# Kernel optimization log

Measured on AMD Instinct MI355X. Metric: run time of the kernel, lower is better.

Reference implementation:

```python
import jax, jax.numpy as jnp
import numpy as np


def setup_inputs() -> dict:
    key = jax.random.key(0)
    ks = jax.random.split(key, 7)
    B, N, F, H = 128, 64, 128, 128
    s1 = 1.0 / np.sqrt(2 * N)  # torch Linear default-ish scaling
    s2 = 1.0 / np.sqrt(H)
    return {
        "agent_features": jax.random.normal(ks[0], (B, N, F), dtype=jnp.float32),
        "W1": jax.random.normal(ks[1], (2 * N, H), dtype=jnp.float32) * s1,
        "b1": jax.random.normal(ks[2], (H,), dtype=jnp.float32) * s1,
        "W2": jax.random.normal(ks[3], (H, H), dtype=jnp.float32) * s2,
        "b2": jax.random.normal(ks[4], (H,), dtype=jnp.float32) * s2,
        "w3": jax.random.normal(ks[5], (H,), dtype=jnp.float32) * s2,
        "b3": jax.random.normal(ks[6], (1,), dtype=jnp.float32) * s2,
        "mixing_weights": jnp.ones((N,), dtype=jnp.float32) / N,
    }


def reference(agent_features, W1, b1, W2, b2, w3, b3, mixing_weights):
    N = mixing_weights.shape[0]
    f = agent_features[:, :, :N]  # [B, N, N] (first num_agents features)
    # Split first Linear's weight into the i-half and j-half of the concat:
    # concat([f_i, f_j]) @ W1 == f_i @ W1[:N] + f_j @ W1[N:]
    Ai = jnp.einsum('bnf,fh->bnh', f, W1[:N])   # contribution of agent i
    Aj = jnp.einsum('bnf,fh->bnh', f, W1[N:])   # contribution of agent j
    h1 = jax.nn.relu(Ai[:, :, None, :] + Aj[:, None, :, :] + b1)  # [B,N,N,H]
    h2 = jax.nn.relu(jnp.einsum('bijh,hk->bijk', h1, W2) + b2)    # [B,N,N,H]
    correlations = jax.nn.sigmoid(jnp.einsum('bijh,h->bij', h2, w3) + b3[0])
    weights = jax.nn.softmax(mixing_weights, axis=0)
    return correlations, weights
```

## Files before the change

### kernel.cpp

```cpp
#include <hip/hip_runtime.h>
#include <hip/hip_bf16.h>


typedef __bf16 bf16x8 __attribute__((ext_vector_type(8)));
typedef float f32x4 __attribute__((ext_vector_type(4)));

__device__ __forceinline__ unsigned rne16(float x) {
  unsigned u = __float_as_uint(x);
  u += 0x7fffu + ((u >> 16) & 1u);
  return u >> 16;
}
__device__ __forceinline__ __bf16 us_as_bf16(unsigned short s) {
  union { unsigned short s; __bf16 h; } cv; cv.s = s; return cv.h;
}

__global__ __launch_bounds__(512, 4) void fused_kernel(
    const float* __restrict__ af, const float* __restrict__ W1,
    const float* __restrict__ b1, const float* __restrict__ W2,
    const float* __restrict__ b2, const float* __restrict__ w3,
    const float* __restrict__ b3, const float* __restrict__ mw,
    float* __restrict__ out)
{
  __shared__ __align__(16) unsigned short W2s[128 * 128];
  __bf16* const flh = (__bf16*)W2s;
  __bf16* const fll = flh + 64 * 72;
  __shared__ __align__(16) float AjF[64 * 132];
  __shared__ __align__(16) float AiF[16 * 132];
  __shared__ float b2s[128], w3s[128];
  __shared__ float part[2][2][128];

  const int tid  = threadIdx.x;
  const int lane = tid & 63;
  const int wave = tid >> 6;
  const int c = lane & 15, g = lane >> 4;
  const int wm = wave & 1;
  const int wn = wave >> 1;

  const int blk = blockIdx.x;
  const int b   = blk >> 2;
  const int iq  = blk & 3;
  const int ip0 = iq << 3;

  if (blk == 0 && tid < 64) {
    float v = mw[tid];
    float m = v;
    for (int off = 32; off > 0; off >>= 1) m = fmaxf(m, __shfl_xor(m, off));
    float e = expf(v - m);
    float s = e;
    for (int off = 32; off > 0; off >>= 1) s += __shfl_xor(s, off);
    out[128 * 64 * 64 + tid] = e / s;
  }

  {
    const float4* srcQ = (const float4*)(af + (b << 13));
#pragma unroll
    for (int p = 0; p < 2; ++p) {
      const int idx = (p << 9) + tid;
      const int n = idx >> 4, e = idx & 15;
      const float4 v = srcQ[(n << 5) + e];
      const unsigned h0 = rne16(v.x), h1 = rne16(v.y),
                     h2 = rne16(v.z), h3 = rne16(v.w);
      const unsigned l0 = rne16(v.x - __uint_as_float(h0 << 16));
      const unsigned l1 = rne16(v.y - __uint_as_float(h1 << 16));
      const unsigned l2 = rne16(v.z - __uint_as_float(h2 << 16));
      const unsigned l3 = rne16(v.w - __uint_as_float(h3 << 16));
      uint2 ph; ph.x = h0 | (h1 << 16); ph.y = h2 | (h3 << 16);
      uint2 pl; pl.x = l0 | (l1 << 16); pl.y = l2 | (l3 << 16);
      *(uint2*)&flh[n * 72 + (e << 2)] = ph;
      *(uint2*)&fll[n * 72 + (e << 2)] = pl;
    }
    if (tid < 128) b2s[tid] = b2[tid];
    else if (tid < 256) w3s[tid - 128] = w3[tid - 128];
  }

  const float bias3 = b3[0];

  __syncthreads();

  {
    const int w = wave;
    bf16x8 ajh[2], ajl[2], aih[2], ail[2];
#pragma unroll
    for (int kc = 0; kc < 2; ++kc) {
      const float* wpj = W1 + ((64 + (kc << 5) + (g << 3)) << 7) + (w << 4) + c;
      const float* wpi = W1 + (((kc << 5) + (g << 3)) << 7) + (w << 4) + c;
#pragma unroll
      for (int e = 0; e < 8; ++e) {
        const float vj = wpj[e << 7];
        const unsigned hj = rne16(vj);
        ajh[kc][e] = us_as_bf16((unsigned short)hj);
        ajl[kc][e] = us_as_bf16((unsigned short)rne16(vj - __uint_as_float(hj << 16)));
        const float vi = wpi[e << 7];
        const unsigned hi_ = rne16(vi);
        aih[kc][e] = us_as_bf16((unsigned short)hi_);
        ail[kc][e] = us_as_bf16((unsigned short)rne16(vi - __uint_as_float(hi_ << 16)));
      }
    }
#pragma unroll
    for (int rt = 0; rt < 4; ++rt) {
      const __bf16* bp = &flh[((rt << 4) + c) * 72 + (g << 3)];
      const __bf16* bq = &fll[((rt << 4) + c) * 72 + (g << 3)];
      f32x4 acc = {0.f, 0.f, 0.f, 0.f};
#pragma unroll
      for (int kc = 0; kc < 2; ++kc) {
        const bf16x8 bh = *(const bf16x8*)(bp + (kc << 5));
        const bf16x8 bl = *(const bf16x8*)(bq + (kc << 5));
        acc = __builtin_amdgcn_mfma_f32_16x16x32_bf16(ajh[kc], bh, acc, 0, 0, 0);
        acc = __builtin_amdgcn_mfma_f32_16x16x32_bf16(ajh[kc], bl, acc, 0, 0, 0);
        acc = __builtin_amdgcn_mfma_f32_16x16x32_bf16(ajl[kc], bh, acc, 0, 0, 0);
      }
      *(f32x4*)&AjF[((rt << 4) + c) * 132 + (w << 4) + (g << 2)] = acc;
    }
    {
      const __bf16* bp = &flh[((iq << 4) + c) * 72 + (g << 3)];
      const __bf16* bq = &fll[((iq << 4) + c) * 72 + (g << 3)];
      f32x4 acc = *(const f32x4*)(b1 + (w << 4) + (g << 2));
#pragma unroll
      for (int kc = 0; kc < 2; ++kc) {
        const bf16x8 bh = *(const bf16x8*)(bp + (kc << 5));
        const bf16x8 bl = *(const bf16x8*)(bq + (kc << 5));
        acc = __builtin_amdgcn_mfma_f32_16x16x32_bf16(aih[kc], bh, acc, 0, 0, 0);
        acc = __builtin_amdgcn_mfma_f32_16x16x32_bf16(aih[kc], bl, acc, 0, 0, 0);
        acc = __builtin_amdgcn_mfma_f32_16x16x32_bf16(ail[kc], bh, acc, 0, 0, 0);
      }
      *(f32x4*)&AiF[c * 132 + (w << 4) + (g << 2)] = acc;
    }
  }

  __syncthreads();

  {
    const int ktw = wn;
#pragma unroll
    for (int mt = 0; mt < 4; ++mt) {
      const int m = (wm << 6) + (mt << 4) + c;
      const float* wp = W2 + (((ktw << 5) + (g << 3)) << 7) + m;
      bf16x8 v;
#pragma unroll
      for (int e = 0; e < 8; ++e) {
        const float vv = wp[e << 7];
        v[e] = us_as_bf16((unsigned short)rne16(vv));
      }
      *(bf16x8*)&W2s[(m << 7) + ((((ktw << 2) + g) ^ c) << 3)] = v;
    }
  }

  f32x4 ajr[4][2][2];
#pragma unroll
  for (int kt = 0; kt < 4; ++kt)
#pragma unroll
    for (int tn = 0; tn < 2; ++tn) {
      const int j = ((wn << 5) + (tn << 4) + c) & 63;
      const float* ajb = &AjF[j * 132 + (g << 3) + (kt << 5)];
      ajr[kt][tn][0] = *(const f32x4*)(ajb);
      ajr[kt][tn][1] = *(const f32x4*)(ajb + 4);
    }

  __syncthreads();

  const int i_sel = wn >> 1;

  for (int t = 0; t < 8; ++t) {
    const float* aib = &AiF[((t << 1) + i_sel) * 132 + (g << 3)];

    f32x4 acc[4][2];
#pragma unroll
    for (int mt = 0; mt < 4; ++mt) {
      const f32x4 bv = *(const f32x4*)&b2s[(wm << 6) + (mt << 4) + (g << 2)];
      acc[mt][0] = bv;
      acc[mt][1] = bv;
    }

#pragma unroll
    for (int kt = 0; kt < 4; ++kt) {
      const int es = ((kt << 2) + g) ^ c;
      bf16x8 wv[4];
#pragma unroll
      for (int mt = 0; mt < 4; ++mt)
        wv[mt] = *(const bf16x8*)&W2s[(((wm << 6) + (mt << 4) + c) << 7) + (es << 3)];

      const f32x4 a0 = *(const f32x4*)(aib + (kt << 5));
      const f32x4 a1 = *(const f32x4*)(aib + (kt << 5) + 4);
      bf16x8 hv[2];
#pragma unroll
      for (int tn = 0; tn < 2; ++tn) {
        const f32x4 h0  = a0 + ajr[kt][tn][0];
        const f32x4 h1v = a1 + ajr[kt][tn][1];
#pragma unroll
        for (int e = 0; e < 4; ++e) {
          hv[tn][e]     = (__bf16)fmaxf(h0[e], 0.f);
          hv[tn][e + 4] = (__bf16)fmaxf(h1v[e], 0.f);
        }
      }
#pragma unroll
      for (int mt = 0; mt < 4; ++mt)
#pragma unroll
        for (int tn = 0; tn < 2; ++tn)
          acc[mt][tn] = __builtin_amdgcn_mfma_f32_16x16x32_bf16(
              wv[mt], hv[tn], acc[mt][tn], 0, 0, 0);
    }

    float s0 = 0.f, s1 = 0.f;
#pragma unroll
    for (int mt = 0; mt < 4; ++mt) {
      const f32x4 wv3 = *(const f32x4*)&w3s[(wm << 6) + (mt << 4) + (g << 2)];
#pragma unroll
      for (int p = 0; p < 4; ++p) {
        s0 = fmaf(fmaxf(acc[mt][0][p], 0.f), wv3[p], s0);
        s1 = fmaf(fmaxf(acc[mt][1][p], 0.f), wv3[p], s1);
      }
    }
    s0 += __shfl_xor(s0, 16);
    s0 += __shfl_xor(s0, 32);
    s1 += __shfl_xor(s1, 16);
    s1 += __shfl_xor(s1, 32);

    const int pb = t & 1;
    if (g == 0) {
      part[pb][wm][(wn << 5) + c]      = s0;
      part[pb][wm][(wn << 5) + 16 + c] = s1;
    }

    __syncthreads();

    if (tid < 128) {
      const float v = part[pb][0][tid] + part[pb][1][tid] + bias3;
      out[(b << 12) + ((ip0 + t) << 7) + tid] = 1.f / (1.f + __expf(-v));
    }
  }
}

extern "C" void kernel_launch(void* const* d_in, const int* in_sizes, int n_in,
                              void* d_out, int out_size, void* d_ws,
                              size_t ws_size, hipStream_t stream)
{
  const float* af = (const float*)d_in[0];
  const float* W1 = (const float*)d_in[1];
  const float* b1 = (const float*)d_in[2];
  const float* W2 = (const float*)d_in[3];
  const float* b2 = (const float*)d_in[4];
  const float* w3 = (const float*)d_in[5];
  const float* b3 = (const float*)d_in[6];
  const float* mw = (const float*)d_in[7];
  float* out = (float*)d_out;

  (void)d_ws; (void)ws_size;
  fused_kernel<<<512, 512, 0, stream>>>(af, W1, b1, W2, b2, w3, b3, mw, out);
}
```

Baseline: 95.32 us.

## Keep W2 fragments in registers and remap waves to process sixteen rows per block

Each wave now holds its bf16 W2 slice (32 output channels across all K tiles) in registers, so the per-iteration LDS reads of W2 and the W2 shared-memory staging are gone. Waves are remapped to a 4×2 split over output channels and columns. Each block walks its 16 i-rows in groups of four, with one barrier and a four-way partial reduction per group, which cuts the number of barriers. The cost is extra register pressure (W2 fragments plus cached Aj values) under the launch bound, which could cause spills or lower occupancy.

```diff
diff --git a/kernel.cpp b/kernel.cpp
--- a/kernel.cpp
+++ b/kernel.cpp
@@ -21,25 +21,25 @@
     const float* __restrict__ b3, const float* __restrict__ mw,
     float* __restrict__ out)
 {
-  __shared__ __align__(16) unsigned short W2s[128 * 128];
-  __bf16* const flh = (__bf16*)W2s;
-  __bf16* const fll = flh + 64 * 72;
+  __shared__ __align__(16) __bf16 flbuf[2 * 64 * 72];
+  __bf16* const flh = flbuf;
+  __bf16* const fll = flbuf + 64 * 72;
   __shared__ __align__(16) float AjF[64 * 132];
   __shared__ __align__(16) float AiF[16 * 132];
   __shared__ float b2s[128], w3s[128];
-  __shared__ float part[2][2][128];
+  __shared__ float part[2][4][4][64];
 
   const int tid  = threadIdx.x;
   const int lane = tid & 63;
   const int wave = tid >> 6;
   const int c = lane & 15, g = lane >> 4;
-  const int wm = wave & 1;
-  const int wn = wave >> 1;
+  const int wm2 = wave & 3;
+  const int wn2 = wave >> 2;
 
   const int blk = blockIdx.x;
   const int b   = blk >> 2;
   const int iq  = blk & 3;
-  const int ip0 = iq << 3;
+  const int i0  = iq << 4;
 
   if (blk == 0 && tid < 64) {
     float v = mw[tid];
@@ -129,103 +129,96 @@
 
   __syncthreads();
 
-  {
-    const int ktw = wn;
-#pragma unroll
-    for (int mt = 0; mt < 4; ++mt) {
-      const int m = (wm << 6) + (mt << 4) + c;
-      const float* wp = W2 + (((ktw << 5) + (g << 3)) << 7) + m;
+  bf16x8 w2r[2][4];
+#pragma unroll
+  for (int mt = 0; mt < 2; ++mt)
+#pragma unroll
+    for (int kt = 0; kt < 4; ++kt) {
+      const int m = (wm2 << 5) + (mt << 4) + c;
+      const float* wp = W2 + (((kt << 5) + (g << 3)) << 7) + m;
       bf16x8 v;
 #pragma unroll
-      for (int e = 0; e < 8; ++e) {
-        const float vv = wp[e << 7];
-        v[e] = us_as_bf16((unsigned short)rne16(vv));
-      }
-      *(bf16x8*)&W2s[(m << 7) + ((((ktw << 2) + g) ^ c) << 3)] = v;
-    }
-  }
+      for (int e = 0; e < 8; ++e)
+        v[e] = us_as_bf16((unsigned short)rne16(wp[e << 7]));
+      w2r[mt][kt] = v;
+    }
 
   f32x4 ajr[4][2][2];
 #pragma unroll
   for (int kt = 0; kt < 4; ++kt)
 #pragma unroll
     for (int tn = 0; tn < 2; ++tn) {
-      const int j = ((wn << 5) + (tn << 4) + c) & 63;
+      const int j = (wn2 << 5) + (tn << 4) + c;
       const float* ajb = &AjF[j * 132 + (g << 3) + (kt << 5)];
       ajr[kt][tn][0] = *(const f32x4*)(ajb);
       ajr[kt][tn][1] = *(const f32x4*)(ajb + 4);
     }
 
-  __syncthreads();
-
-  const int i_sel = wn >> 1;
-
-  for (int t = 0; t < 8; ++t) {
-    const float* aib = &AiF[((t << 1) + i_sel) * 132 + (g << 3)];
-
-    f32x4 acc[4][2];
-#pragma unroll
-    for (int mt = 0; mt < 4; ++mt) {
-      const f32x4 bv = *(const f32x4*)&b2s[(wm << 6) + (mt << 4) + (g << 2)];
-      acc[mt][0] = bv;
-      acc[mt][1] = bv;
-    }
-
-#pragma unroll
-    for (int kt = 0; kt < 4; ++kt) {
-      const int es = ((kt << 2) + g) ^ c;
-      bf16x8 wv[4];
-#pragma unroll
-      for (int mt = 0; mt < 4; ++mt)
-        wv[mt] = *(const bf16x8*)&W2s[(((wm << 6) + (mt << 4) + c) << 7) + (es << 3)];
-
-      const f32x4 a0 = *(const f32x4*)(aib + (kt << 5));
-      const f32x4 a1 = *(const f32x4*)(aib + (kt << 5) + 4);
-      bf16x8 hv[2];
-#pragma unroll
-      for (int tn = 0; tn < 2; ++tn) {
-        const f32x4 h0  = a0 + ajr[kt][tn][0];
-        const f32x4 h1v = a1 + ajr[kt][tn][1];
-#pragma unroll
-        for (int e = 0; e < 4; ++e) {
-          hv[tn][e]     = (__bf16)fmaxf(h0[e], 0.f);
-          hv[tn][e + 4] = (__bf16)fmaxf(h1v[e], 0.f);
+  for (int bt = 0; bt < 4; ++bt) {
+    for (int tt = 0; tt < 4; ++tt) {
+      const int tp = (bt << 2) + tt;
+      const float* aib = &AiF[tp * 132 + (g << 3)];
+
+      f32x4 acc[2][2];
+#pragma unroll
+      for (int mt = 0; mt < 2; ++mt) {
+        const f32x4 bv = *(const f32x4*)&b2s[(wm2 << 5) + (mt << 4) + (g << 2)];
+        acc[mt][0] = bv;
+        acc[mt][1] = bv;
+      }
+
+#pragma unroll
+      for (int kt = 0; kt < 4; ++kt) {
+        const f32x4 a0 = *(const f32x4*)(aib + (kt << 5));
+        const f32x4 a1 = *(const f32x4*)(aib + (kt << 5) + 4);
+        bf16x8 hv[2];
+#pragma unroll
+        for (int tn = 0; tn < 2; ++tn) {
+          const f32x4 h0  = a0 + ajr[kt][tn][0];
+          const f32x4 h1v = a1 + ajr[kt][tn][1];
+#pragma unroll
+          for (int e = 0; e < 4; ++e) {
+            hv[tn][e]     = (__bf16)fmaxf(h0[e], 0.f);
+            hv[tn][e + 4] = (__bf16)fmaxf(h1v[e], 0.f);
+          }
         }
-      }
-#pragma unroll
-      for (int mt = 0; mt < 4; ++mt)
-#pragma unroll
-        for (int tn = 0; tn < 2; ++tn)
-          acc[mt][tn] = __builtin_amdgcn_mfma_f32_16x16x32_bf16(
-              wv[mt], hv[tn], acc[mt][tn], 0, 0, 0);
-    }
-
-    float s0 = 0.f, s1 = 0.f;
-#pragma unroll
-    for (int mt = 0; mt < 4; ++mt) {
-      const f32x4 wv3 = *(const f32x4*)&w3s[(wm << 6) + (mt << 4) + (g << 2)];
-#pragma unroll
-      for (int p = 0; p < 4; ++p) {
-        s0 = fmaf(fmaxf(acc[mt][0][p], 0.f), wv3[p], s0);
-        s1 = fmaf(fmaxf(acc[mt][1][p], 0.f), wv3[p], s1);
-      }
-    }
-    s0 += __shfl_xor(s0, 16);
-    s0 += __shfl_xor(s0, 32);
-    s1 += __shfl_xor(s1, 16);
-    s1 += __shfl_xor(s1, 32);
-
-    const int pb = t & 1;
-    if (g == 0) {
-      part[pb][wm][(wn << 5) + c]      = s0;
-      part[pb][wm][(wn << 5) + 16 + c] = s1;
+#pragma unroll
+        for (int mt = 0; mt < 2; ++mt)
+#pragma unroll
+          for (int tn = 0; tn < 2; ++tn)
+            acc[mt][tn] = __builtin_amdgcn_mfma_f32_16x16x32_bf16(
+                w2r[mt][kt], hv[tn], acc[mt][tn], 0, 0, 0);
+      }
+
+      float s0 = 0.f, s1 = 0.f;
+#pragma unroll
+      for (int mt = 0; mt < 2; ++mt) {
+        const f32x4 wv3 = *(const f32x4*)&w3s[(wm2 << 5) + (mt << 4) + (g << 2)];
+#pragma unroll
+        for (int p = 0; p < 4; ++p) {
+          s0 = fmaf(fmaxf(acc[mt][0][p], 0.f), wv3[p], s0);
+          s1 = fmaf(fmaxf(acc[mt][1][p], 0.f), wv3[p], s1);
+        }
+      }
+      s0 += __shfl_xor(s0, 16);
+      s0 += __shfl_xor(s0, 32);
+      s1 += __shfl_xor(s1, 16);
+      s1 += __shfl_xor(s1, 32);
+
+      if (g == 0) {
+        part[bt & 1][tt][wm2][(wn2 << 5) + c]      = s0;
+        part[bt & 1][tt][wm2][(wn2 << 5) + 16 + c] = s1;
+      }
     }
 
     __syncthreads();
 
-    if (tid < 128) {
-      const float v = part[pb][0][tid] + part[pb][1][tid] + bias3;
-      out[(b << 12) + ((ip0 + t) << 7) + tid] = 1.f / (1.f + __expf(-v));
+    if (tid < 256) {
+      const int tt = tid >> 6, j = tid & 63;
+      const float v = part[bt & 1][tt][0][j] + part[bt & 1][tt][1][j] +
+                      part[bt & 1][tt][2][j] + part[bt & 1][tt][3][j] + bias3;
+      out[(b << 12) + ((i0 + (bt << 2) + tt) << 6) + j] =
+          1.f / (1.f + __expf(-v));
     }
   }
 }
```

Measured after the change: 170.4 us. 1.79x slower.
